# Kernel optimization log

Hardware: AMD Instinct MI355X
Metric: run time of the kernel (lower is better)

Reference implementation:

```python
import jax, jax.numpy as jnp
import numpy as np

N, E, D, H, L = 50000, 800000, 64, 4, 2
DH = D // H


def layer_norm(h, g, b, eps=1e-5):
    mu = h.mean(-1, keepdims=True)
    var = ((h - mu) ** 2).mean(-1, keepdims=True)
    return (h - mu) / jnp.sqrt(var + eps) * g + b


def setup_inputs() -> dict:
    key = jax.random.key(0)
    ks = jax.random.split(key, 16)
    s = 1.0 / np.sqrt(D)
    inp = {
        "x": jax.random.normal(ks[0], (N, D), jnp.float32),
        "edge_attr": jax.random.normal(ks[1], (E, D), jnp.float32),
        "edge_index": jax.random.randint(ks[2], (2, E), 0, N, jnp.int64),
        "WQ": jax.random.normal(ks[3], (L, D, D), jnp.float32) * s,
        "WK": jax.random.normal(ks[4], (L, D, D), jnp.float32) * s,
        "WE": jax.random.normal(ks[5], (L, D, D), jnp.float32) * s,
        "WV": jax.random.normal(ks[6], (L, D, D), jnp.float32) * s,
        "WO": jax.random.normal(ks[7], (L, D, D), jnp.float32) * s,
        "bO": jnp.zeros((L, D), jnp.float32),
        "ln1_g": jnp.ones((L, D), jnp.float32),
        "ln1_b": jnp.zeros((L, D), jnp.float32),
        "W1": jax.random.normal(ks[8], (L, D, 2 * D), jnp.float32) * s,
        "b1": jnp.zeros((L, 2 * D), jnp.float32),
        "W2": jax.random.normal(ks[9], (L, 2 * D, D), jnp.float32) * (1.0 / np.sqrt(2 * D)),
        "b2": jnp.zeros((L, D), jnp.float32),
        "ln2_g": jnp.ones((L, D), jnp.float32),
        "ln2_b": jnp.zeros((L, D), jnp.float32),
    }
    return inp


def exphormer_layer(h, edge_attr, src, dst, p):
    (wq, wk, we, wv, wo, bo, g1, be1, w1, b1, w2, b2, g2, be2) = p
    n = h.shape[0]
    Qh = (h @ wq).reshape(n, H, DH)
    Kh = (h @ wk).reshape(n, H, DH)
    Vh = (h @ wv).reshape(n, H, DH)
    Eh = (edge_attr @ we).reshape(-1, H, DH)
    # per-edge score: sum over head_dim of K[src]*Q[dst]*E / sqrt(DH)
    s = jnp.sum(Kh[src] * Qh[dst] * Eh, axis=-1, keepdims=True) / np.sqrt(DH)
    score = jnp.exp(jnp.clip(s, -5.0, 5.0))  # [E, H, 1]
    msg = Vh[src] * score                     # [E, H, DH]
    wV = jax.ops.segment_sum(msg, dst, num_segments=n)    # [N, H, DH]
    Z = jax.ops.segment_sum(score, dst, num_segments=n)   # [N, H, 1]
    h_attn = (wV / (Z + 1e-6)).reshape(n, D)
    h1 = layer_norm(h + (h_attn @ wo + bo), g1, be1)
    ffn = jax.nn.relu(h1 @ w1 + b1) @ w2 + b2
    return layer_norm(h1 + ffn, g2, be2)


def reference(x, edge_attr, edge_index, WQ, WK, WE, WV, WO, bO, ln1_g, ln1_b,
              W1, b1, W2, b2, ln2_g, ln2_b):
    src = edge_index[0]
    dst = edge_index[1]
    h = x
    for l in range(L):
        p = (WQ[l], WK[l], WE[l], WV[l], WO[l], bO[l], ln1_g[l], ln1_b[l],
             W1[l], b1[l], W2[l], b2[l], ln2_g[l], ln2_b[l])
        h = exphormer_layer(h, edge_attr, src, dst, p)
    return h
```

## Files before the change

kernel.cpp:

```cpp
#include <hip/hip_runtime.h>

#define NN 50000
#define NE 800000
#define D  64
#define NL 2

typedef __bf16 bf16x8 __attribute__((ext_vector_type(8)));
typedef float  floatx4 __attribute__((ext_vector_type(4)));

static __device__ __forceinline__ float bf2f(unsigned short u) {
    return __uint_as_float(((unsigned)u) << 16);
}
static __device__ __forceinline__ unsigned short f2bf(float x) {
    unsigned u = __float_as_uint(x);
    u += 0x7fff + ((u >> 16) & 1);
    return (unsigned short)(u >> 16);
}


__global__ void k_deg(const int* __restrict__ ei, int* __restrict__ deg) {
    int e = blockIdx.x * 256 + threadIdx.x;
    if (e < NE) atomicAdd(&deg[ei[NE + e]], 1);
}

__global__ void k_scan(const int* __restrict__ deg, int* __restrict__ row_off,
                       int* __restrict__ cursor) {
    __shared__ int buf[1024];
    __shared__ int carry_s;
    if (threadIdx.x == 0) carry_s = 0;
    __syncthreads();
    for (int base = 0; base < NN; base += 1024) {
        int i = base + (int)threadIdx.x;
        int v = (i < NN) ? deg[i] : 0;
        buf[threadIdx.x] = v;
        __syncthreads();
        for (int offt = 1; offt < 1024; offt <<= 1) {
            int t = (threadIdx.x >= (unsigned)offt) ? buf[threadIdx.x - offt] : 0;
            __syncthreads();
            buf[threadIdx.x] += t;
            __syncthreads();
        }
        int inc = buf[threadIdx.x] + carry_s;
        if (i < NN) {
            row_off[i + 1] = inc;
            cursor[i] = inc - v;
            if (i == 0) row_off[0] = 0;
        }
        __syncthreads();
        if (threadIdx.x == 1023) carry_s = inc;
        __syncthreads();
    }
}

__global__ void k_scatter(const int* __restrict__ ei, int* __restrict__ cursor,
                          int* __restrict__ csr_src, int* __restrict__ eperm) {
    int e = blockIdx.x * 256 + threadIdx.x;
    if (e < NE) {
        int dst = ei[NE + e];
        int pos = atomicAdd(&cursor[dst], 1);
        csr_src[pos] = ei[e];
        eperm[e] = pos;
    }
}

__global__ __launch_bounds__(256) void k_prep(
        const float* __restrict__ WQ, const float* __restrict__ WK,
        const float* __restrict__ WV, const float* __restrict__ WE,
        const float* __restrict__ WO, const float* __restrict__ W1,
        const float* __restrict__ W2,
        unsigned short* __restrict__ wqT, unsigned short* __restrict__ wkT,
        unsigned short* __restrict__ wvT, unsigned short* __restrict__ weT,
        unsigned short* __restrict__ woT, unsigned short* __restrict__ w1T,
        unsigned short* __restrict__ w2T) {
    int idx = blockIdx.x * 256 + threadIdx.x;
    if (idx >= 2 * 36864) return;
    int l = idx / 36864;
    int r = idx % 36864;
    if (r < 20480) {
        int which = r >> 12, rr = r & 4095;
        int m = rr >> 6, k = rr & 63;
        const float* src = (which == 0 ? WQ : which == 1 ? WK : which == 2 ? WV :
                            which == 3 ? WE : WO);
        unsigned short* dst = (which == 0 ? wqT : which == 1 ? wkT : which == 2 ? wvT :
                               which == 3 ? weT : woT);
        dst[l * 4096 + rr] = f2bf(src[l * 4096 + k * 64 + m]);
    } else if (r < 28672) {
        int r2 = r - 20480;
        int m = r2 >> 6, k = r2 & 63;
        w1T[l * 8192 + r2] = f2bf(W1[l * 8192 + k * 128 + m]);
    } else {
        int r3 = r - 28672;
        int m = r3 >> 7, k = r3 & 127;
        w2T[l * 8192 + r3] = f2bf(W2[l * 8192 + k * 64 + m]);
    }
}


__global__ __launch_bounds__(256) void k_qkv_mfma(const float* __restrict__ h,
        const unsigned short* __restrict__ wqT, const unsigned short* __restrict__ wkT,
        const unsigned short* __restrict__ wvT,
        float* __restrict__ Qh, unsigned short* __restrict__ Kb,
        unsigned short* __restrict__ Vb) {
    __shared__ unsigned short st[4][16 * 72];
    const int lane = threadIdx.x & 63;
    const int w    = threadIdx.x >> 6;
    const int ml   = lane & 15;
    const int quad = lane >> 4;

    bf16x8 aq[2][4], ak[2][4], av[2][4];
#pragma unroll
    for (int kt = 0; kt < 2; kt++)
#pragma unroll
        for (int mt = 0; mt < 4; mt++) {
            int o = (mt*16 + ml)*64 + kt*32 + quad*8;
            aq[kt][mt] = *(const bf16x8*)&wqT[o];
            ak[kt][mt] = *(const bf16x8*)&wkT[o];
            av[kt][mt] = *(const bf16x8*)&wvT[o];
        }

    const int wave = blockIdx.x * 4 + w;
    const int nw   = gridDim.x * 4;
    for (int tile = wave; tile < NN / 16; tile += nw) {
        const int e0 = tile * 16;
        const float4* ar = (const float4*)(h + (size_t)(e0 + ml) * D);
        bf16x8 b[2];
#pragma unroll
        for (int kt = 0; kt < 2; kt++) {
            float4 f0 = ar[kt*8 + quad*2 + 0];
            float4 f1 = ar[kt*8 + quad*2 + 1];
            b[kt][0] = (__bf16)f0.x; b[kt][1] = (__bf16)f0.y;
            b[kt][2] = (__bf16)f0.z; b[kt][3] = (__bf16)f0.w;
            b[kt][4] = (__bf16)f1.x; b[kt][5] = (__bf16)f1.y;
            b[kt][6] = (__bf16)f1.z; b[kt][7] = (__bf16)f1.w;
        }
        floatx4 accq[4] = {}, acck[4] = {}, accv[4] = {};
#pragma unroll
        for (int kt = 0; kt < 2; kt++)
#pragma unroll
            for (int mt = 0; mt < 4; mt++) {
                accq[mt] = __builtin_amdgcn_mfma_f32_16x16x32_bf16(aq[kt][mt], b[kt], accq[mt], 0, 0, 0);
                acck[mt] = __builtin_amdgcn_mfma_f32_16x16x32_bf16(ak[kt][mt], b[kt], acck[mt], 0, 0, 0);
                accv[mt] = __builtin_amdgcn_mfma_f32_16x16x32_bf16(av[kt][mt], b[kt], accv[mt], 0, 0, 0);
            }
#pragma unroll
        for (int mt = 0; mt < 4; mt++)
            *(float4*)(Qh + (size_t)(e0 + ml) * D + mt*16 + quad*4) =
                make_float4(accq[mt][0], accq[mt][1], accq[mt][2], accq[mt][3]);
        const int el = lane >> 2, c = lane & 3;
#pragma unroll
        for (int mt = 0; mt < 4; mt++)
            *(ushort4*)&st[w][ml*72 + mt*16 + quad*4] =
                make_ushort4(f2bf(acck[mt][0]), f2bf(acck[mt][1]),
                             f2bf(acck[mt][2]), f2bf(acck[mt][3]));
        {
            uint4 r0 = *(const uint4*)&st[w][el*72 + c*16 + 0];
            uint4 r1 = *(const uint4*)&st[w][el*72 + c*16 + 8];
            uint4* gp = (uint4*)(Kb + (size_t)(e0 + el) * D + c*16);
            gp[0] = r0; gp[1] = r1;
        }
#pragma unroll
        for (int mt = 0; mt < 4; mt++)
            *(ushort4*)&st[w][ml*72 + mt*16 + quad*4] =
                make_ushort4(f2bf(accv[mt][0]), f2bf(accv[mt][1]),
                             f2bf(accv[mt][2]), f2bf(accv[mt][3]));
        {
            uint4 r0 = *(const uint4*)&st[w][el*72 + c*16 + 0];
            uint4 r1 = *(const uint4*)&st[w][el*72 + c*16 + 8];
            uint4* gp = (uint4*)(Vb + (size_t)(e0 + el) * D + c*16);
            gp[0] = r0; gp[1] = r1;
        }
    }
}

__global__ __launch_bounds__(256) void k_eh_mfma(const float* __restrict__ ea,
        const unsigned short* __restrict__ weT, const int* __restrict__ eperm,
        unsigned short* __restrict__ Eh) {
    __shared__ unsigned short st[4][16 * 72];
    const int lane = threadIdx.x & 63;
    const int w    = threadIdx.x >> 6;
    const int ml   = lane & 15;
    const int quad = lane >> 4;

    bf16x8 afr[2][4];
#pragma unroll
    for (int kt = 0; kt < 2; kt++)
#pragma unroll
        for (int mt = 0; mt < 4; mt++)
            afr[kt][mt] = *(const bf16x8*)&weT[(mt*16 + ml)*64 + kt*32 + quad*8];

    const int wave = blockIdx.x * 4 + w;
    const int nw   = gridDim.x * 4;
    for (int tile = wave; tile < NE / 16; tile += nw) {
        const int e0 = tile * 16;
        const float4* ar = (const float4*)(ea + (size_t)(e0 + ml) * D);
        floatx4 acc[4] = {};
#pragma unroll
        for (int kt = 0; kt < 2; kt++) {
            float4 f0 = ar[kt*8 + quad*2 + 0];
            float4 f1 = ar[kt*8 + quad*2 + 1];
            bf16x8 b;
            b[0] = (__bf16)f0.x; b[1] = (__bf16)f0.y; b[2] = (__bf16)f0.z; b[3] = (__bf16)f0.w;
            b[4] = (__bf16)f1.x; b[5] = (__bf16)f1.y; b[6] = (__bf16)f1.z; b[7] = (__bf16)f1.w;
#pragma unroll
            for (int mt = 0; mt < 4; mt++)
                acc[mt] = __builtin_amdgcn_mfma_f32_16x16x32_bf16(afr[kt][mt], b, acc[mt], 0, 0, 0);
        }
#pragma unroll
        for (int mt = 0; mt < 4; mt++)
            *(ushort4*)&st[w][ml*72 + mt*16 + quad*4] =
                make_ushort4(f2bf(acc[mt][0]), f2bf(acc[mt][1]),
                             f2bf(acc[mt][2]), f2bf(acc[mt][3]));
        const int el = lane >> 2, c = lane & 3;
        int pos = eperm[e0 + el];
        uint4 r0 = *(const uint4*)&st[w][el*72 + c*16 + 0];
        uint4 r1 = *(const uint4*)&st[w][el*72 + c*16 + 8];
        uint4* gp = (uint4*)(Eh + (size_t)pos * D + c*16);
        gp[0] = r0;
        gp[1] = r1;
    }
}

__global__ __launch_bounds__(256) void k_agg(const float* __restrict__ Qh,
        const unsigned short* __restrict__ Kb, const unsigned short* __restrict__ Vb,
        const unsigned short* __restrict__ Eh,
        const int* __restrict__ row_off, const int* __restrict__ csr_src,
        float* __restrict__ h_attn) {
    int t = blockIdx.x * 256 + threadIdx.x;
    int node = t >> 4;
    int lane = t & 15;
    if (node >= NN) return;
    int beg = row_off[node], end = row_off[node + 1];
    float4 q = ((const float4*)(Qh + (size_t)node * D))[lane];
    float4 acc = make_float4(0.f, 0.f, 0.f, 0.f);
    float z = 0.f;
    for (int i = beg; i < end; i++) {
        int s = csr_src[i];
        ushort4 kb = *(const ushort4*)(Kb + (size_t)s * D + lane * 4);
        ushort4 eb = *(const ushort4*)(Eh + (size_t)i * D + lane * 4);
        float part = bf2f(kb.x) * q.x * bf2f(eb.x) + bf2f(kb.y) * q.y * bf2f(eb.y)
                   + bf2f(kb.z) * q.z * bf2f(eb.z) + bf2f(kb.w) * q.w * bf2f(eb.w);
        part += __shfl_xor(part, 1, 64);
        part += __shfl_xor(part, 2, 64);
        float sv = part * 0.25f;
        sv = fminf(5.f, fmaxf(-5.f, sv));
        float sc = __expf(sv);
        ushort4 vb = *(const ushort4*)(Vb + (size_t)s * D + lane * 4);
        acc.x += sc * bf2f(vb.x); acc.y += sc * bf2f(vb.y);
        acc.z += sc * bf2f(vb.z); acc.w += sc * bf2f(vb.w);
        z += sc;
    }
    float inv = 1.f / (z + 1e-6f);
    ((float4*)(h_attn + (size_t)node * D))[lane] =
        make_float4(acc.x * inv, acc.y * inv, acc.z * inv, acc.w * inv);
}

__global__ __launch_bounds__(512) void k_post_mfma(const float* __restrict__ h_in,
        const float* __restrict__ h_attn,
        const unsigned short* __restrict__ woT_g,
        const unsigned short* __restrict__ w1T_g,
        const unsigned short* __restrict__ w2T_g,
        const float* __restrict__ bo,
        const float* __restrict__ g1, const float* __restrict__ be1,
        const float* __restrict__ b1, const float* __restrict__ b2,
        const float* __restrict__ g2, const float* __restrict__ be2,
        float* __restrict__ h_out) {
    __shared__ unsigned short woT_s[64 * 72];
    __shared__ unsigned short w1T_s[128 * 72];
    __shared__ unsigned short w2T_s[64 * 136];
    __shared__ unsigned short stg[8][16 * 136];

    const int t = threadIdx.x;
    {
        const uint4* s0 = (const uint4*)woT_g;
        { int i = t; if (i < 512) { int row = i >> 3, c = i & 7;
              *(uint4*)&woT_s[row*72 + c*8] = s0[i]; } }
        const uint4* s1 = (const uint4*)w1T_g;
        for (int i = t; i < 1024; i += 512) {
            int row = i >> 3, c = i & 7;
            *(uint4*)&w1T_s[row*72 + c*8] = s1[i];
        }
        const uint4* s2 = (const uint4*)w2T_g;
        for (int i = t; i < 1024; i += 512) {
            int row = i >> 4, c = i & 15;
            *(uint4*)&w2T_s[row*136 + c*8] = s2[i];
        }
    }
    __syncthreads();

    const int w = t >> 6, lane = t & 63;
    const int ml = lane & 15, quad = lane >> 4;
    const int tile = blockIdx.x * 8 + w;
    if (tile >= NN / 16) return;
    const int e0 = tile * 16;
    unsigned short* st = stg[w];

    const float4* ap = (const float4*)(h_attn + (size_t)(e0 + ml) * D);
    floatx4 acc1[4] = {};
#pragma unroll
    for (int kt = 0; kt < 2; kt++) {
        float4 f0 = ap[kt*8 + quad*2 + 0];
        float4 f1 = ap[kt*8 + quad*2 + 1];
        bf16x8 b;
        b[0] = (__bf16)f0.x; b[1] = (__bf16)f0.y; b[2] = (__bf16)f0.z; b[3] = (__bf16)f0.w;
        b[4] = (__bf16)f1.x; b[5] = (__bf16)f1.y; b[6] = (__bf16)f1.z; b[7] = (__bf16)f1.w;
#pragma unroll
        for (int mt = 0; mt < 4; mt++) {
            bf16x8 a = *(const bf16x8*)&woT_s[(mt*16 + ml)*72 + kt*32 + quad*8];
            acc1[mt] = __builtin_amdgcn_mfma_f32_16x16x32_bf16(a, b, acc1[mt], 0, 0, 0);
        }
    }
    const float4* hp  = (const float4*)(h_in + (size_t)(e0 + ml) * D);
    const float4* bo4 = (const float4*)bo;
    floatx4 tt[4];
#pragma unroll
    for (int mt = 0; mt < 4; mt++) {
        float4 hh = hp[mt*4 + quad];
        float4 bb = bo4[mt*4 + quad];
        tt[mt][0] = acc1[mt][0] + hh.x + bb.x;
        tt[mt][1] = acc1[mt][1] + hh.y + bb.y;
        tt[mt][2] = acc1[mt][2] + hh.z + bb.z;
        tt[mt][3] = acc1[mt][3] + hh.w + bb.w;
    }
    float s = 0.f;
#pragma unroll
    for (int mt = 0; mt < 4; mt++) s += tt[mt][0] + tt[mt][1] + tt[mt][2] + tt[mt][3];
    s += __shfl_xor(s, 16, 64); s += __shfl_xor(s, 32, 64);
    float mu = s * (1.f / 64.f);
    float v = 0.f;
#pragma unroll
    for (int mt = 0; mt < 4; mt++)
#pragma unroll
        for (int r = 0; r < 4; r++) { float c = tt[mt][r] - mu; v += c * c; }
    v += __shfl_xor(v, 16, 64); v += __shfl_xor(v, 32, 64);
    float rstd = rsqrtf(v * (1.f / 64.f) + 1e-5f);
    const float4* g1v  = (const float4*)g1;
    const float4* be1v = (const float4*)be1;
    floatx4 h1[4];
#pragma unroll
    for (int mt = 0; mt < 4; mt++) {
        float4 gg = g1v[mt*4 + quad];
        float4 bb = be1v[mt*4 + quad];
        h1[mt][0] = (tt[mt][0] - mu) * rstd * gg.x + bb.x;
        h1[mt][1] = (tt[mt][1] - mu) * rstd * gg.y + bb.y;
        h1[mt][2] = (tt[mt][2] - mu) * rstd * gg.z + bb.z;
        h1[mt][3] = (tt[mt][3] - mu) * rstd * gg.w + bb.w;
        *(ushort4*)&st[ml*136 + mt*16 + quad*4] =
            make_ushort4(f2bf(h1[mt][0]), f2bf(h1[mt][1]), f2bf(h1[mt][2]), f2bf(h1[mt][3]));
    }

    bf16x8 bh[2];
#pragma unroll
    for (int kt = 0; kt < 2; kt++)
        bh[kt] = *(const bf16x8*)&st[ml*136 + kt*32 + quad*8];
    floatx4 acc2[8] = {};
#pragma unroll
    for (int kt = 0; kt < 2; kt++)
#pragma unroll
        for (int mt = 0; mt < 8; mt++) {
            bf16x8 a = *(const bf16x8*)&w1T_s[(mt*16 + ml)*72 + kt*32 + quad*8];
            acc2[mt] = __builtin_amdgcn_mfma_f32_16x16x32_bf16(a, bh[kt], acc2[mt], 0, 0, 0);
        }
    const float4* b1v = (const float4*)b1;
#pragma unroll
    for (int mt = 0; mt < 8; mt++) {
        float4 bb = b1v[mt*4 + quad];
        float y0 = fmaxf(acc2[mt][0] + bb.x, 0.f);
        float y1 = fmaxf(acc2[mt][1] + bb.y, 0.f);
        float y2 = fmaxf(acc2[mt][2] + bb.z, 0.f);
        float y3 = fmaxf(acc2[mt][3] + bb.w, 0.f);
        *(ushort4*)&st[ml*136 + mt*16 + quad*4] =
            make_ushort4(f2bf(y0), f2bf(y1), f2bf(y2), f2bf(y3));
    }

    floatx4 acc3[4] = {};
#pragma unroll
    for (int kt = 0; kt < 4; kt++) {
        bf16x8 b = *(const bf16x8*)&st[ml*136 + kt*32 + quad*8];
#pragma unroll
        for (int mt = 0; mt < 4; mt++) {
            bf16x8 a = *(const bf16x8*)&w2T_s[(mt*16 + ml)*136 + kt*32 + quad*8];
            acc3[mt] = __builtin_amdgcn_mfma_f32_16x16x32_bf16(a, b, acc3[mt], 0, 0, 0);
        }
    }
    const float4* b2v = (const float4*)b2;
#pragma unroll
    for (int mt = 0; mt < 4; mt++) {
        float4 bb = b2v[mt*4 + quad];
        tt[mt][0] = acc3[mt][0] + bb.x + h1[mt][0];
        tt[mt][1] = acc3[mt][1] + bb.y + h1[mt][1];
        tt[mt][2] = acc3[mt][2] + bb.z + h1[mt][2];
        tt[mt][3] = acc3[mt][3] + bb.w + h1[mt][3];
    }
    s = 0.f;
#pragma unroll
    for (int mt = 0; mt < 4; mt++) s += tt[mt][0] + tt[mt][1] + tt[mt][2] + tt[mt][3];
    s += __shfl_xor(s, 16, 64); s += __shfl_xor(s, 32, 64);
    mu = s * (1.f / 64.f);
    v = 0.f;
#pragma unroll
    for (int mt = 0; mt < 4; mt++)
#pragma unroll
        for (int r = 0; r < 4; r++) { float c = tt[mt][r] - mu; v += c * c; }
    v += __shfl_xor(v, 16, 64); v += __shfl_xor(v, 32, 64);
    rstd = rsqrtf(v * (1.f / 64.f) + 1e-5f);
    const float4* g2v  = (const float4*)g2;
    const float4* be2v = (const float4*)be2;
    float4* outp = (float4*)(h_out + (size_t)(e0 + ml) * D);
#pragma unroll
    for (int mt = 0; mt < 4; mt++) {
        float4 gg = g2v[mt*4 + quad];
        float4 bb = be2v[mt*4 + quad];
        float4 o;
        o.x = (tt[mt][0] - mu) * rstd * gg.x + bb.x;
        o.y = (tt[mt][1] - mu) * rstd * gg.y + bb.y;
        o.z = (tt[mt][2] - mu) * rstd * gg.z + bb.z;
        o.w = (tt[mt][3] - mu) * rstd * gg.w + bb.w;
        outp[mt*4 + quad] = o;
    }
}


extern "C" void kernel_launch(void* const* d_in, const int* in_sizes, int n_in,
                              void* d_out, int out_size, void* d_ws, size_t ws_size,
                              hipStream_t stream) {
    const float* x   = (const float*)d_in[0];
    const float* ea  = (const float*)d_in[1];
    const int*   ei  = (const int*)d_in[2];
    const float* WQ  = (const float*)d_in[3];
    const float* WK  = (const float*)d_in[4];
    const float* WE  = (const float*)d_in[5];
    const float* WV  = (const float*)d_in[6];
    const float* WO  = (const float*)d_in[7];
    const float* bO  = (const float*)d_in[8];
    const float* g1  = (const float*)d_in[9];
    const float* be1 = (const float*)d_in[10];
    const float* W1  = (const float*)d_in[11];
    const float* b1  = (const float*)d_in[12];
    const float* W2  = (const float*)d_in[13];
    const float* b2  = (const float*)d_in[14];
    const float* g2  = (const float*)d_in[15];
    const float* be2 = (const float*)d_in[16];
    float* out = (float*)d_out;

    char* wsb = (char*)d_ws;
    size_t off = 0;
    auto alloc = [&](size_t bytes) {
        void* p = wsb + off;
        off += (bytes + 255) & ~(size_t)255;
        return p;
    };
    float* Qh            = (float*)alloc((size_t)NN * D * 4);
    unsigned short* Kb   = (unsigned short*)alloc((size_t)NN * D * 2);
    unsigned short* Vb   = (unsigned short*)alloc((size_t)NN * D * 2);
    float* hbuf          = (float*)alloc((size_t)NN * D * 4);
    float* hattn         = (float*)alloc((size_t)NN * D * 4);
    unsigned short* Eh   = (unsigned short*)alloc((size_t)NE * D * 2);
    int* row_off         = (int*)alloc((size_t)(NN + 1) * 4);
    int* cursor          = (int*)alloc((size_t)NN * 4);
    int* deg             = (int*)alloc((size_t)NN * 4);
    int* csr_src         = (int*)alloc((size_t)NE * 4);
    int* eperm           = (int*)alloc((size_t)NE * 4);
    unsigned short* wqT  = (unsigned short*)alloc((size_t)2 * 4096 * 2);
    unsigned short* wkT  = (unsigned short*)alloc((size_t)2 * 4096 * 2);
    unsigned short* wvT  = (unsigned short*)alloc((size_t)2 * 4096 * 2);
    unsigned short* weT  = (unsigned short*)alloc((size_t)2 * 4096 * 2);
    unsigned short* woT  = (unsigned short*)alloc((size_t)2 * 4096 * 2);
    unsigned short* w1T  = (unsigned short*)alloc((size_t)2 * 8192 * 2);
    unsigned short* w2T  = (unsigned short*)alloc((size_t)2 * 8192 * 2);

    hipMemsetAsync(deg, 0, (size_t)NN * 4, stream);
    k_deg<<<(NE + 255) / 256, 256, 0, stream>>>(ei, deg);
    k_scan<<<1, 1024, 0, stream>>>(deg, row_off, cursor);
    k_scatter<<<(NE + 255) / 256, 256, 0, stream>>>(ei, cursor, csr_src, eperm);
    k_prep<<<(2 * 36864 + 255) / 256, 256, 0, stream>>>(WQ, WK, WV, WE, WO, W1, W2,
            wqT, wkT, wvT, weT, woT, w1T, w2T);

    for (int l = 0; l < NL; l++) {
        const float* hcur = (l == 0) ? x : hbuf;
        float* hnxt = (l == NL - 1) ? out : hbuf;
        k_qkv_mfma<<<256, 256, 0, stream>>>(hcur, wqT + l * 4096, wkT + l * 4096,
                                            wvT + l * 4096, Qh, Kb, Vb);
        k_eh_mfma<<<1024, 256, 0, stream>>>(ea, weT + l * 4096, eperm, Eh);
        k_agg<<<(NN * 16 + 255) / 256, 256, 0, stream>>>(Qh, Kb, Vb, Eh, row_off, csr_src, hattn);
        k_post_mfma<<<(NN / 16 + 7) / 8, 512, 0, stream>>>(hcur, hattn,
                woT + l * 4096, w1T + l * 8192, w2T + l * 8192,
                bO + l * 64, g1 + l * 64, be1 + l * 64,
                b1 + l * 128, b2 + l * 64,
                g2 + l * 64, be2 + l * 64, hnxt);
    }
}
```

Before: 746.9 us.

## Hoist edge projection for both layers into one pass; parallelize aggregation per wave

The edge-attribute projection now runs once before the layer loop. It reads edge_attr a single time and writes bf16 Eh for both layers into a doubled buffer. The aggregation kernel now assigns one 64-lane wave per node instead of 16 lanes, so four edges are processed concurrently and two are loaded per iteration, with a cross-slot shuffle reduction at the end. This is meant to raise memory-level parallelism on the gathers. The QKV grid size also grows from 256 to 782 blocks. The cost is extra workspace for the second Eh copy and idle lanes on low-degree nodes.

```diff
diff --git a/kernel.cpp b/kernel.cpp
--- a/kernel.cpp
+++ b/kernel.cpp
@@ -181,42 +181,51 @@
     const int ml   = lane & 15;
     const int quad = lane >> 4;
 
-    bf16x8 afr[2][4];
-#pragma unroll
-    for (int kt = 0; kt < 2; kt++)
-#pragma unroll
-        for (int mt = 0; mt < 4; mt++)
-            afr[kt][mt] = *(const bf16x8*)&weT[(mt*16 + ml)*64 + kt*32 + quad*8];
+    bf16x8 afr[2][2][4];
+#pragma unroll
+    for (int l = 0; l < 2; l++)
+#pragma unroll
+        for (int kt = 0; kt < 2; kt++)
+#pragma unroll
+            for (int mt = 0; mt < 4; mt++)
+                afr[l][kt][mt] = *(const bf16x8*)&weT[l*4096 + (mt*16 + ml)*64 + kt*32 + quad*8];
 
     const int wave = blockIdx.x * 4 + w;
     const int nw   = gridDim.x * 4;
+    const int el = lane >> 2, c = lane & 3;
     for (int tile = wave; tile < NE / 16; tile += nw) {
         const int e0 = tile * 16;
         const float4* ar = (const float4*)(ea + (size_t)(e0 + ml) * D);
-        floatx4 acc[4] = {};
+        bf16x8 b[2];
 #pragma unroll
         for (int kt = 0; kt < 2; kt++) {
             float4 f0 = ar[kt*8 + quad*2 + 0];
             float4 f1 = ar[kt*8 + quad*2 + 1];
-            bf16x8 b;
-            b[0] = (__bf16)f0.x; b[1] = (__bf16)f0.y; b[2] = (__bf16)f0.z; b[3] = (__bf16)f0.w;
-            b[4] = (__bf16)f1.x; b[5] = (__bf16)f1.y; b[6] = (__bf16)f1.z; b[7] = (__bf16)f1.w;
+            b[kt][0] = (__bf16)f0.x; b[kt][1] = (__bf16)f0.y;
+            b[kt][2] = (__bf16)f0.z; b[kt][3] = (__bf16)f0.w;
+            b[kt][4] = (__bf16)f1.x; b[kt][5] = (__bf16)f1.y;
+            b[kt][6] = (__bf16)f1.z; b[kt][7] = (__bf16)f1.w;
+        }
+        int pos = eperm[e0 + el];
+#pragma unroll
+        for (int l = 0; l < 2; l++) {
+            floatx4 acc[4] = {};
+#pragma unroll
+            for (int kt = 0; kt < 2; kt++)
+#pragma unroll
+                for (int mt = 0; mt < 4; mt++)
+                    acc[mt] = __builtin_amdgcn_mfma_f32_16x16x32_bf16(afr[l][kt][mt], b[kt], acc[mt], 0, 0, 0);
 #pragma unroll
             for (int mt = 0; mt < 4; mt++)
-                acc[mt] = __builtin_amdgcn_mfma_f32_16x16x32_bf16(afr[kt][mt], b, acc[mt], 0, 0, 0);
-        }
-#pragma unroll
-        for (int mt = 0; mt < 4; mt++)
-            *(ushort4*)&st[w][ml*72 + mt*16 + quad*4] =
-                make_ushort4(f2bf(acc[mt][0]), f2bf(acc[mt][1]),
-                             f2bf(acc[mt][2]), f2bf(acc[mt][3]));
-        const int el = lane >> 2, c = lane & 3;
-        int pos = eperm[e0 + el];
-        uint4 r0 = *(const uint4*)&st[w][el*72 + c*16 + 0];
-        uint4 r1 = *(const uint4*)&st[w][el*72 + c*16 + 8];
-        uint4* gp = (uint4*)(Eh + (size_t)pos * D + c*16);
-        gp[0] = r0;
-        gp[1] = r1;
+                *(ushort4*)&st[w][ml*72 + mt*16 + quad*4] =
+                    make_ushort4(f2bf(acc[mt][0]), f2bf(acc[mt][1]),
+                                 f2bf(acc[mt][2]), f2bf(acc[mt][3]));
+            uint4 r0 = *(const uint4*)&st[w][el*72 + c*16 + 0];
+            uint4 r1 = *(const uint4*)&st[w][el*72 + c*16 + 8];
+            uint4* gp = (uint4*)(Eh + (size_t)l * NE * D + (size_t)pos * D + c*16);
+            gp[0] = r0;
+            gp[1] = r1;
+        }
     }
 }
 
@@ -225,33 +234,61 @@
         const unsigned short* __restrict__ Eh,
         const int* __restrict__ row_off, const int* __restrict__ csr_src,
         float* __restrict__ h_attn) {
-    int t = blockIdx.x * 256 + threadIdx.x;
-    int node = t >> 4;
-    int lane = t & 15;
+    const int node = blockIdx.x * 4 + (threadIdx.x >> 6);
     if (node >= NN) return;
-    int beg = row_off[node], end = row_off[node + 1];
-    float4 q = ((const float4*)(Qh + (size_t)node * D))[lane];
+    const int lane  = threadIdx.x & 63;
+    const int eslot = lane >> 4;
+    const int ml    = lane & 15;
+    const int beg = row_off[node], end = row_off[node + 1];
+    const float4 q = ((const float4*)(Qh + (size_t)node * D))[ml];
     float4 acc = make_float4(0.f, 0.f, 0.f, 0.f);
     float z = 0.f;
-    for (int i = beg; i < end; i++) {
-        int s = csr_src[i];
-        ushort4 kb = *(const ushort4*)(Kb + (size_t)s * D + lane * 4);
-        ushort4 eb = *(const ushort4*)(Eh + (size_t)i * D + lane * 4);
-        float part = bf2f(kb.x) * q.x * bf2f(eb.x) + bf2f(kb.y) * q.y * bf2f(eb.y)
-                   + bf2f(kb.z) * q.z * bf2f(eb.z) + bf2f(kb.w) * q.w * bf2f(eb.w);
-        part += __shfl_xor(part, 1, 64);
-        part += __shfl_xor(part, 2, 64);
-        float sv = part * 0.25f;
-        sv = fminf(5.f, fmaxf(-5.f, sv));
-        float sc = __expf(sv);
-        ushort4 vb = *(const ushort4*)(Vb + (size_t)s * D + lane * 4);
-        acc.x += sc * bf2f(vb.x); acc.y += sc * bf2f(vb.y);
-        acc.z += sc * bf2f(vb.z); acc.w += sc * bf2f(vb.w);
-        z += sc;
-    }
-    float inv = 1.f / (z + 1e-6f);
-    ((float4*)(h_attn + (size_t)node * D))[lane] =
-        make_float4(acc.x * inv, acc.y * inv, acc.z * inv, acc.w * inv);
+
+    int i0 = beg + eslot;
+    while (i0 < end) {
+        int i1 = i0 + 4;
+        bool a1 = i1 < end;
+        int s0 = csr_src[i0];
+        int p1 = a1 ? i1 : i0;
+        int s1 = a1 ? csr_src[p1] : s0;
+        ushort4 kb0 = *(const ushort4*)(Kb + (size_t)s0 * D + ml * 4);
+        ushort4 eb0 = *(const ushort4*)(Eh + (size_t)i0 * D + ml * 4);
+        ushort4 vb0 = *(const ushort4*)(Vb + (size_t)s0 * D + ml * 4);
+        ushort4 kb1 = *(const ushort4*)(Kb + (size_t)s1 * D + ml * 4);
+        ushort4 eb1 = *(const ushort4*)(Eh + (size_t)p1 * D + ml * 4);
+        ushort4 vb1 = *(const ushort4*)(Vb + (size_t)s1 * D + ml * 4);
+
+        float part0 = bf2f(kb0.x) * q.x * bf2f(eb0.x) + bf2f(kb0.y) * q.y * bf2f(eb0.y)
+                    + bf2f(kb0.z) * q.z * bf2f(eb0.z) + bf2f(kb0.w) * q.w * bf2f(eb0.w);
+        float part1 = bf2f(kb1.x) * q.x * bf2f(eb1.x) + bf2f(kb1.y) * q.y * bf2f(eb1.y)
+                    + bf2f(kb1.z) * q.z * bf2f(eb1.z) + bf2f(kb1.w) * q.w * bf2f(eb1.w);
+        part0 += __shfl_xor(part0, 1, 64);
+        part0 += __shfl_xor(part0, 2, 64);
+        part1 += __shfl_xor(part1, 1, 64);
+        part1 += __shfl_xor(part1, 2, 64);
+        float sc0 = __expf(fminf(5.f, fmaxf(-5.f, part0 * 0.25f)));
+        float sc1 = a1 ? __expf(fminf(5.f, fmaxf(-5.f, part1 * 0.25f))) : 0.f;
+
+        acc.x += sc0 * bf2f(vb0.x) + sc1 * bf2f(vb1.x);
+        acc.y += sc0 * bf2f(vb0.y) + sc1 * bf2f(vb1.y);
+        acc.z += sc0 * bf2f(vb0.z) + sc1 * bf2f(vb1.z);
+        acc.w += sc0 * bf2f(vb0.w) + sc1 * bf2f(vb1.w);
+        z += sc0 + sc1;
+        i0 += 8;
+    }
+#pragma unroll
+    for (int m = 16; m <= 32; m <<= 1) {
+        acc.x += __shfl_xor(acc.x, m, 64);
+        acc.y += __shfl_xor(acc.y, m, 64);
+        acc.z += __shfl_xor(acc.z, m, 64);
+        acc.w += __shfl_xor(acc.w, m, 64);
+        z     += __shfl_xor(z, m, 64);
+    }
+    if (eslot == 0) {
+        float inv = 1.f / (z + 1e-6f);
+        ((float4*)(h_attn + (size_t)node * D))[ml] =
+            make_float4(acc.x * inv, acc.y * inv, acc.z * inv, acc.w * inv);
+    }
 }
 
 __global__ __launch_bounds__(512) void k_post_mfma(const float* __restrict__ h_in,
@@ -454,7 +491,7 @@
     unsigned short* Vb   = (unsigned short*)alloc((size_t)NN * D * 2);
     float* hbuf          = (float*)alloc((size_t)NN * D * 4);
     float* hattn         = (float*)alloc((size_t)NN * D * 4);
-    unsigned short* Eh   = (unsigned short*)alloc((size_t)NE * D * 2);
+    unsigned short* Eh   = (unsigned short*)alloc((size_t)NL * NE * D * 2);
     int* row_off         = (int*)alloc((size_t)(NN + 1) * 4);
     int* cursor          = (int*)alloc((size_t)NN * 4);
     int* deg             = (int*)alloc((size_t)NN * 4);
@@ -474,14 +511,15 @@
     k_scatter<<<(NE + 255) / 256, 256, 0, stream>>>(ei, cursor, csr_src, eperm);
     k_prep<<<(2 * 36864 + 255) / 256, 256, 0, stream>>>(WQ, WK, WV, WE, WO, W1, W2,
             wqT, wkT, wvT, weT, woT, w1T, w2T);
+    k_eh_mfma<<<1024, 256, 0, stream>>>(ea, weT, eperm, Eh);
 
     for (int l = 0; l < NL; l++) {
         const float* hcur = (l == 0) ? x : hbuf;
         float* hnxt = (l == NL - 1) ? out : hbuf;
-        k_qkv_mfma<<<256, 256, 0, stream>>>(hcur, wqT + l * 4096, wkT + l * 4096,
+        k_qkv_mfma<<<782, 256, 0, stream>>>(hcur, wqT + l * 4096, wkT + l * 4096,
                                             wvT + l * 4096, Qh, Kb, Vb);
-        k_eh_mfma<<<1024, 256, 0, stream>>>(ea, weT + l * 4096, eperm, Eh);
-        k_agg<<<(NN * 16 + 255) / 256, 256, 0, stream>>>(Qh, Kb, Vb, Eh, row_off, csr_src, hattn);
+        k_agg<<<(NN + 3) / 4, 256, 0, stream>>>(Qh, Kb, Vb, Eh + (size_t)l * NE * D,
+                                                row_off, csr_src, hattn);
         k_post_mfma<<<(NN / 16 + 7) / 8, 512, 0, stream>>>(hcur, hattn,
                 woT + l * 4096, w1T + l * 8192, w2T + l * 8192,
                 bO + l * 64, g1 + l * 64, be1 + l * 64,
```

New measurement: 717.7 us. 1.04x faster.
